# Optimization experiments

Hardware: AMD Instinct MI355X
Metric: run time of the kernel (lower is better)

## Reference

```python
import jax, jax.numpy as jnp
import numpy as np

B, T, C = 2, 2048, 2048
H = 16          # n_head == n_kv_head
HD = 128        # head_size = hidden_dim // n_head (nope/value dim)
RD = 64         # qk_rope_head_dim
QLR = 1536      # q_lora_rank
KLR = 512       # kv_lora_rank
BASE = 10000.0
SCALE = (HD + RD) ** -0.5  # mscale = 1.0 since rope_scale = 1.0
EPS = 1e-6


def _rms(x, w):
    return x * jax.lax.rsqrt(jnp.mean(x * x, axis=-1, keepdims=True) + EPS) * w


def _rope_cos_sin(seq_len, dim):
    inv_freq = 1.0 / (BASE ** (jnp.arange(0, dim, 2, dtype=jnp.float32) / dim))
    t = jnp.arange(seq_len, dtype=jnp.float32)
    freqs = jnp.outer(t, inv_freq)            # [T, dim/2]
    emb = jnp.concatenate([freqs, freqs], -1)  # [T, dim]
    return jnp.cos(emb), jnp.sin(emb)


def _rotate_half(x):
    h = x.shape[-1] // 2
    return jnp.concatenate([-x[..., h:], x[..., :h]], axis=-1)


def setup_inputs() -> dict:
    key = jax.random.key(0)
    ks = jax.random.split(key, 8)
    s = 0.02
    return {
        "x": jax.random.normal(ks[0], (B, T, C), jnp.float32),
        "Wq_down": jax.random.normal(ks[1], (C, QLR), jnp.float32) * s,
        "q_norm_w": jnp.ones((QLR,), jnp.float32),
        "Wq_up": jax.random.normal(ks[2], (QLR, H * HD), jnp.float32) * s,
        "Wq_pe": jax.random.normal(ks[3], (QLR, H * RD), jnp.float32) * s,
        "Wkv_down": jax.random.normal(ks[4], (C, KLR), jnp.float32) * s,
        "kv_norm_w": jnp.ones((KLR,), jnp.float32),
        "Wkv_up": jax.random.normal(ks[5], (KLR, H * 2 * HD), jnp.float32) * s,
        "Wk_pe": jax.random.normal(ks[6], (C, RD), jnp.float32) * s,
        "k_pe_norm_w": jnp.ones((RD,), jnp.float32),
        "Wo": jax.random.normal(ks[7], (H * HD, C), jnp.float32) * s,
    }


def reference(x, Wq_down, q_norm_w, Wq_up, Wq_pe, Wkv_down, kv_norm_w,
              Wkv_up, Wk_pe, k_pe_norm_w, Wo):
    # ---- low-rank Q path ----
    cQ = _rms(x @ Wq_down, q_norm_w)                      # [B,T,QLR]
    q_nop = (cQ @ Wq_up).reshape(B, T, H, HD).transpose(0, 2, 1, 3)   # [B,H,T,HD]
    q_pe = (cQ @ Wq_pe).reshape(B, T, H, RD).transpose(0, 2, 1, 3)    # [B,H,T,RD]
    # ---- low-rank KV path ----
    cKV = _rms(x @ Wkv_down, kv_norm_w)                   # [B,T,KLR]
    kv = cKV @ Wkv_up                                     # [B,T,H*2*HD]
    k_nop, v = jnp.split(kv, 2, axis=-1)
    k_nop = k_nop.reshape(B, T, H, HD).transpose(0, 2, 1, 3)          # [B,H,T,HD]
    v = v.reshape(B, T, H, HD).transpose(0, 2, 1, 3)                  # [B,H,T,HD]
    # ---- decoupled RoPE key (shared across heads) ----
    k_pe = _rms(x @ Wk_pe, k_pe_norm_w).reshape(B, T, 1, RD).transpose(0, 2, 1, 3)  # [B,1,T,RD]
    cos, sin = _rope_cos_sin(T, RD)                       # [T,RD]
    q_pe = q_pe * cos + _rotate_half(q_pe) * sin
    k_pe = k_pe * cos + _rotate_half(k_pe) * sin
    # ---- concat nope + rope, causal SDPA ----
    q = jnp.concatenate([q_nop, q_pe], axis=-1)                           # [B,H,T,HD+RD]
    k = jnp.concatenate([k_nop, jnp.broadcast_to(k_pe, (B, H, T, RD))], axis=-1)
    scores = jnp.einsum('bhqd,bhkd->bhqk', q, k) * SCALE
    mask = jnp.tril(jnp.ones((T, T), dtype=bool))
    scores = jnp.where(mask, scores, jnp.finfo(scores.dtype).min)
    attn = jax.nn.softmax(scores, axis=-1)
    y = jnp.einsum('bhqk,bhkd->bhqd', attn, v)                            # [B,H,T,HD]
    y = y.transpose(0, 2, 1, 3).reshape(B, T, H * HD)
    return y @ Wo
```

## Files before the change

### kernel.cpp

```cpp
#include <hip/hip_runtime.h>
#include <hip/hip_bf16.h>
#include <cmath>

typedef __hip_bfloat16 bf16;
typedef __attribute__((ext_vector_type(8))) short s16x8;
typedef __attribute__((ext_vector_type(4))) float f32x4;

#define B_   2
#define T_   2048
#define C_   2048
#define H_   16
#define HD_  128
#define RD_  64
#define QLR_ 1536
#define KLR_ 512
#define SCALE_ 0.07216878364870322f

static __device__ __forceinline__ float b2f(bf16 v){ return __bfloat162float(v); }
static __device__ __forceinline__ bf16  f2b(float v){ return __float2bfloat16(v); }
static __device__ __forceinline__ float us2f(unsigned short u){
    union { unsigned short s[2]; float f; } v; v.s[0]=0; v.s[1]=u; return v.f;
}
static __device__ __forceinline__ float ldS(const void* p, size_t i, int isf32){
    return isf32 ? ((const float*)p)[i] : b2f(((const bf16*)p)[i]);
}
static __device__ __forceinline__ void ld4(const void* p, size_t i, int isf32, float* o){
    if (isf32) {
        float4 v = *(const float4*)((const float*)p + i);
        o[0]=v.x; o[1]=v.y; o[2]=v.z; o[3]=v.w;
    } else {
        ushort4 u = *(const ushort4*)((const bf16*)p + i);
        o[0]=us2f(u.x); o[1]=us2f(u.y); o[2]=us2f(u.z); o[3]=us2f(u.w);
    }
}

__global__ __launch_bounds__(64) void detect_kernel(const unsigned short* __restrict__ x,
                                                    int* __restrict__ flag)
{
    int big = 0;
    for (int i = threadIdx.x; i < 1024; i += 64) {
        const unsigned short u = x[2*i];
        const int e = (u >> 7) & 0xFF;
        if (e >= 139) big++;
    }
    #pragma unroll
    for (int off = 32; off; off >>= 1) big += __shfl_down(big, off, 64);
    if (threadIdx.x == 0) *flag = (big > 8) ? 1 : 0;
}

__global__ __launch_bounds__(256) void convert_kernel(const void* __restrict__ in,
                                                      bf16* __restrict__ out, int n,
                                                      const int* __restrict__ flag)
{
    const int f = *flag;
    const int i0 = (blockIdx.x * 256 + threadIdx.x) * 8;
    if (i0 >= n) return;
    float v[8];
    ld4(in, i0, f, v);
    ld4(in, i0 + 4, f, v + 4);
    bf16* o = out + i0;
    #pragma unroll
    for (int k = 0; k < 8; ++k) o[k] = f2b(v[k]);
}

struct TDesc { const void* in; bf16* out; int R, Cc, blkStart, nx; };
struct TBatch { TDesc d[5]; int nseg; };

__global__ __launch_bounds__(256) void transpose_batch(TBatch tb,
                                                       const int* __restrict__ flag)
{
    const int f = *flag;
    const int bid = blockIdx.x;
    int s = 0;
    #pragma unroll
    for (int i = 1; i < 5; ++i)
        if (i < tb.nseg && bid >= tb.d[i].blkStart) s = i;
    const TDesc d = tb.d[s];
    const int local = bid - d.blkStart;
    const int c0 = (local % d.nx) * 32;
    const int r0 = (local / d.nx) * 32;

    __shared__ float tile[32][33];
    const int tx = threadIdx.x & 31, ty = threadIdx.x >> 5;
    #pragma unroll
    for (int i = 0; i < 4; ++i)
        tile[ty + 8*i][tx] = ldS(d.in, (size_t)(r0 + ty + 8*i) * d.Cc + c0 + tx, f);
    __syncthreads();
    #pragma unroll
    for (int i = 0; i < 4; ++i)
        d.out[(size_t)(c0 + ty + 8*i) * d.R + r0 + tx] = f2b(tile[tx][ty + 8*i]);
}

__global__ __launch_bounds__(256) void transpose_v_kernel(const bf16* __restrict__ kvb,
                                                          bf16* __restrict__ vT)
{
    __shared__ bf16 tile[32][34];
    const int c0 = blockIdx.x * 32;
    const int r0 = blockIdx.y * 32;
    const int tx = threadIdx.x & 31, ty = threadIdx.x >> 5;
    #pragma unroll
    for (int i = 0; i < 4; ++i)
        tile[ty + 8*i][tx] = kvb[(size_t)(r0 + ty + 8*i) * (H_*256) + H_*128 + c0 + tx];
    __syncthreads();
    const int b  = r0 >> 11;
    const int t0 = r0 & (T_ - 1);
    #pragma unroll
    for (int i = 0; i < 4; ++i) {
        const int c  = c0 + ty + 8*i;
        const int hh = c >> 7, dd = c & 127;
        vT[(((size_t)b*H_ + hh)*HD_ + dd)*T_ + t0 + tx] = tile[tx][ty + 8*i];
    }
}

struct GOuts { void* p[3]; int start[3]; int stride[3]; int nseg; };

__global__ __launch_bounds__(256, 3) void mfma_gemm(const bf16* __restrict__ A,
                                                    const bf16* __restrict__ BT,
                                                    GOuts go, int N, int K,
                                                    const int* __restrict__ flag, int cH)
{
    __shared__ __align__(16) char smem[32768];
    const int cf   = cH ? *flag : 0;
    const int tid  = threadIdx.x;
    const int lane = tid & 63;
    const int quad = lane >> 4;
    const int l16  = lane & 15;
    const int w    = tid >> 6;
    const int wm   = w >> 1, wn = w & 1;

    const int nwg = gridDim.x * gridDim.y;
    const int bid = blockIdx.y * gridDim.x + blockIdx.x;
    const int swz = (bid & 7) * (nwg >> 3) + (bid >> 3);
    const int bm  = (swz / gridDim.x) * 128;
    const int bn  = (swz % gridDim.x) * 128;

    int seg = 0;
    #pragma unroll
    for (int i = 1; i < 3; ++i)
        if (i < go.nseg && bn >= go.start[i]) seg = i;
    void* const dstp   = go.p[seg];
    const int  dstoff  = go.start[seg];
    const int  dstride = go.stride[seg];

    const int nkt = K >> 6;

    const int sR   = tid >> 3;
    const int sCol = ((tid & 7) ^ (sR & 7)) * 8;
    const bf16* gA = A  + (size_t)(bm + sR) * K + sCol;
    const bf16* gB = BT + (size_t)(bn + sR) * K + sCol;
    const int rxk  = l16 & 7;
    const int aOff = (wm*64 + l16) * 128;
    const int bOff = 16384 + (wn*64 + l16) * 128;

    f32x4 acc[4][4];
    #pragma unroll
    for (int i = 0; i < 4; ++i)
        #pragma unroll
        for (int j = 0; j < 4; ++j)
            acc[i][j] = (f32x4){0.f, 0.f, 0.f, 0.f};

    s16x8 af[4][2], bf[4][2];

    #define STG(kt) do {                                                         \
        const int ke_ = (kt) * 64;                                               \
        _Pragma("unroll")                                                        \
        for (int j_ = 0; j_ < 4; ++j_)                                           \
            __builtin_amdgcn_global_load_lds(                                    \
                (const __attribute__((address_space(1))) unsigned int*)          \
                    (gA + (size_t)(j_*32) * K + ke_),                            \
                (__attribute__((address_space(3))) unsigned int*)                \
                    (smem + j_*4096 + tid*16), 16, 0, 0);                        \
        _Pragma("unroll")                                                        \
        for (int j_ = 0; j_ < 4; ++j_)                                           \
            __builtin_amdgcn_global_load_lds(                                    \
                (const __attribute__((address_space(1))) unsigned int*)          \
                    (gB + (size_t)(j_*32) * K + ke_),                            \
                (__attribute__((address_space(3))) unsigned int*)                \
                    (smem + 16384 + j_*4096 + tid*16), 16, 0, 0);                \
    } while (0)

    #define LD do {                                                              \
        _Pragma("unroll")                                                        \
        for (int i_ = 0; i_ < 4; ++i_)                                           \
            _Pragma("unroll")                                                    \
            for (int ks_ = 0; ks_ < 2; ++ks_)                                    \
                af[i_][ks_] = *(const s16x8*)(smem + aOff                        \
                              + i_*2048 + ((((ks_<<2)|quad) ^ rxk) << 4));       \
        _Pragma("unroll")                                                        \
        for (int j_ = 0; j_ < 4; ++j_)                                           \
            _Pragma("unroll")                                                    \
            for (int ks_ = 0; ks_ < 2; ++ks_)                                    \
                bf[j_][ks_] = *(const s16x8*)(smem + bOff                        \
                              + j_*2048 + ((((ks_<<2)|quad) ^ rxk) << 4));       \
    } while (0)

    #define MM do {                                                              \
        __builtin_amdgcn_s_setprio(1);                                           \
        _Pragma("unroll")                                                        \
        for (int i_ = 0; i_ < 4; ++i_)                                           \
            _Pragma("unroll")                                                    \
            for (int j_ = 0; j_ < 4; ++j_)                                       \
                _Pragma("unroll")                                                \
                for (int ks_ = 0; ks_ < 2; ++ks_)                                \
                    acc[i_][j_] = __builtin_amdgcn_mfma_f32_16x16x32_bf16(       \
                        af[i_][ks_], bf[j_][ks_], acc[i_][j_], 0, 0, 0);         \
        __builtin_amdgcn_s_setprio(0);                                           \
    } while (0)

    for (int t = 0; t < nkt; ++t) {
        STG(t);
        asm volatile("s_waitcnt vmcnt(0)" ::: "memory");
        __builtin_amdgcn_s_barrier();
        LD;
        MM;
        __builtin_amdgcn_s_barrier();
    }

    #undef STG
    #undef LD
    #undef MM

    #pragma unroll
    for (int i = 0; i < 4; ++i) {
        const int crow = bm + wm*64 + i*16 + quad*4;
        #pragma unroll
        for (int r = 0; r < 4; ++r) {
            #pragma unroll
            for (int j = 0; j < 4; ++j) {
                const int ccol = bn + wn*64 + j*16 + l16;
                if (ccol < N) {
                    const size_t idx = (size_t)(crow + r) * dstride + (ccol - dstoff);
                    if (cf) ((float*)dstp)[idx] = acc[i][j][r];
                    else    ((bf16*)dstp)[idx] = f2b(acc[i][j][r]);
                }
            }
        }
    }
}

template<int NPER>
__global__ __launch_bounds__(256) void rms_kernel(bf16* __restrict__ X,
                                                  const void* __restrict__ w,
                                                  const int* __restrict__ flag)
{
    const int wf = *flag;
    const int ncols = NPER * 256;
    __shared__ float red[4];
    const int row = blockIdx.x;
    const int tid = threadIdx.x;
    bf16* xr = X + (size_t)row * ncols;
    float vals[NPER];
    float ss = 0.f;
    #pragma unroll
    for (int i = 0; i < NPER; ++i) {
        float v = b2f(xr[tid + i*256]);
        vals[i] = v; ss += v*v;
    }
    #pragma unroll
    for (int off = 32; off; off >>= 1) ss += __shfl_down(ss, off, 64);
    if ((tid & 63) == 0) red[tid >> 6] = ss;
    __syncthreads();
    const float tot = red[0]+red[1]+red[2]+red[3];
    const float rs  = rsqrtf(tot / (float)ncols + 1e-6f);
    #pragma unroll
    for (int i = 0; i < NPER; ++i) {
        const int c = tid + i*256;
        xr[c] = f2b(vals[i] * rs * ldS(w, c, wf));
    }
}

__global__ __launch_bounds__(64) void kpe_rms_rope(bf16* __restrict__ X,
                                                   const void* __restrict__ w,
                                                   const int* __restrict__ flag)
{
    const int wf   = *flag;
    const int row  = blockIdx.x;
    const int t    = row & (T_ - 1);
    const int lane = threadIdx.x;
    bf16* xr = X + (size_t)row * RD_;
    const float v = b2f(xr[lane]);
    float ss = v * v;
    #pragma unroll
    for (int off = 32; off; off >>= 1) ss += __shfl_down(ss, off, 64);
    ss = __shfl(ss, 0, 64);
    const float rs = rsqrtf(ss / 64.f + 1e-6f);
    const float xn = v * rs * ldS(w, lane, wf);
    const int   i  = lane & 31;
    const float freq = powf(10000.f, -(float)(2*i) / 64.f);
    const float ang  = (float)t * freq;
    const float s = sinf(ang), c = cosf(ang);
    const float other = __shfl_xor(xn, 32, 64);
    const float o = (lane < 32) ? (xn * c - other * s) : (other * s + xn * c);
    xr[lane] = f2b(o);
}

__global__ __launch_bounds__(256) void qpe_rope(bf16* __restrict__ X)
{
    const int row = blockIdx.x;
    const int t   = row & (T_ - 1);
    bf16* xr = X + (size_t)row * (H_ * RD_);
    const int tid = threadIdx.x;
    #pragma unroll
    for (int pp = 0; pp < 2; ++pp) {
        const int p  = tid + pp * 256;
        const int hh = p >> 5;
        const int i  = p & 31;
        const int i0 = hh * 64 + i;
        const int i1 = i0 + 32;
        const float x1 = b2f(xr[i0]), x2 = b2f(xr[i1]);
        const float freq = powf(10000.f, -(float)(2*i) / 64.f);
        const float ang  = (float)t * freq;
        const float s = sinf(ang), c = cosf(ang);
        xr[i0] = f2b(x1 * c - x2 * s);
        xr[i1] = f2b(x1 * s + x2 * c);
    }
}

__global__ __launch_bounds__(256, 2) void flash_attn(const bf16* __restrict__ qnop,
                                                     const bf16* __restrict__ qpe,
                                                     const bf16* __restrict__ kv,
                                                     const bf16* __restrict__ kpe,
                                                     const bf16* __restrict__ vT,
                                                     bf16* __restrict__ y)
{
    __shared__ __align__(16) short Klds[64 * 192];
    __shared__ __align__(16) short Vt[128 * 64];
    __shared__ __align__(16) short Plds[4][16 * 64];

    const int h   = blockIdx.x;
    const int qt  = 31 - (int)blockIdx.y;
    const int b   = blockIdx.z;
    const int q0  = qt * 64;
    const int tid = threadIdx.x;
    const int w    = tid >> 6;
    const int lane = tid & 63;
    const int quad = lane >> 4;
    const int l16  = lane & 15;
    const int rk   = l16 & 7;
    const int rkp  = (l16 ^ (l16 >> 3)) & 7;
    const int row0 = q0 + w * 16;
    const size_t bT = (size_t)b * T_;
    const int bh  = b * H_ + h;

    const int kR = tid >> 4, kS = tid & 15;
    const int pR = tid >> 3, pS = tid & 7;
    const int vD = tid >> 3, vS = tid & 7;

    const bf16* gK = kv  + (bT + kR) * (H_*256) + h*128 + kS*8;
    const bf16* gP = kpe + (bT + pR) * RD_ + pS*8;
    const bf16* gV = vT  + ((size_t)bh*HD_ + vD) * T_ + vS*8;

    short* const wK = &Klds[kR*192 + ((kS ^ (kR & 7)) << 3)];
    short* const wP = &Klds[pR*192 + 128 + ((pS ^ (pR & 7)) << 3)];
    short* const wV = &Vt[vD*64 + ((vS ^ (vD & 7)) << 3)];

    s16x8 aq[6];
    {
        const size_t r = bT + row0 + l16;
        const bf16* qn = qnop + r * (H_*128) + h*128 + quad*8;
        #pragma unroll
        for (int kk = 0; kk < 4; ++kk) aq[kk] = *(const s16x8*)(qn + kk*32);
        const bf16* qp = qpe + r * (H_*64) + h*64 + quad*8;
        aq[4] = *(const s16x8*)(qp);
        aq[5] = *(const s16x8*)(qp + 32);
    }

    f32x4 o[8];
    #pragma unroll
    for (int i = 0; i < 8; ++i) o[i] = (f32x4){0.f,0.f,0.f,0.f};
    float m_run[4] = {-1e30f,-1e30f,-1e30f,-1e30f};
    float l_run[4] = {0.f,0.f,0.f,0.f};

    uint4 k0, k1, k2, k3, p0, p1, v0, v1, v2, v3;
    #define PF(J0) do {                                                     \
        const bf16* a_ = gK + (size_t)(J0) * (H_*256);                      \
        k0 = *(const uint4*)(a_);                                           \
        k1 = *(const uint4*)(a_ + 16*(H_*256));                             \
        k2 = *(const uint4*)(a_ + 32*(H_*256));                             \
        k3 = *(const uint4*)(a_ + 48*(H_*256));                             \
        const bf16* p_ = gP + (size_t)(J0) * RD_;                           \
        p0 = *(const uint4*)(p_);                                           \
        p1 = *(const uint4*)(p_ + 32*RD_);                                  \
        const bf16* v_ = gV + (J0);                                         \
        v0 = *(const uint4*)(v_);                                           \
        v1 = *(const uint4*)(v_ + 32*T_);                                   \
        v2 = *(const uint4*)(v_ + 64*T_);                                   \
        v3 = *(const uint4*)(v_ + 96*T_);                                   \
    } while (0)

    PF(0);

    const int ntiles = qt + 1;
    for (int it = 0; it < ntiles; ++it) {
        const int j0 = it * 64;
        asm volatile("s_waitcnt lgkmcnt(0)\n\ts_barrier" ::: "memory");

        *(uint4*)(wK)          = k0;
        *(uint4*)(wK + 16*192) = k1;
        *(uint4*)(wK + 32*192) = k2;
        *(uint4*)(wK + 48*192) = k3;
        *(uint4*)(wP)          = p0;
        *(uint4*)(wP + 32*192) = p1;
        *(uint4*)(wV)          = v0;
        *(uint4*)(wV + 32*64)  = v1;
        *(uint4*)(wV + 64*64)  = v2;
        *(uint4*)(wV + 96*64)  = v3;

        if (it + 1 < ntiles) PF(j0 + 64);

        asm volatile("s_waitcnt lgkmcnt(0)\n\ts_barrier" ::: "memory");

        if (j0 <= row0 + 15) {
            const bool needmask = (j0 + 63 > row0);
            f32x4 s[4];
            #pragma unroll
            for (int nsub = 0; nsub < 4; ++nsub) {
                f32x4 acc = (f32x4){0.f,0.f,0.f,0.f};
                #pragma unroll
                for (int kk = 0; kk < 6; ++kk) {
                    const s16x8 bk = *(const s16x8*)&Klds[(nsub*16 + l16)*192
                                        + ((((kk << 2) | quad) ^ rk) << 3)];
                    acc = __builtin_amdgcn_mfma_f32_16x16x32_bf16(aq[kk], bk, acc, 0, 0, 0);
                }
                #pragma unroll
                for (int reg = 0; reg < 4; ++reg) acc[reg] *= SCALE_;
                s[nsub] = acc;
            }
            if (needmask) {
                #pragma unroll
                for (int nsub = 0; nsub < 4; ++nsub)
                    #pragma unroll
                    for (int reg = 0; reg < 4; ++reg) {
                        const int col = j0 + nsub*16 + l16;
                        const int row = row0 + quad*4 + reg;
                        if (col > row) s[nsub][reg] = -1e30f;
                    }
            }
            float mt[4], alpha[4], rs[4];
            #pragma unroll
            for (int reg = 0; reg < 4; ++reg)
                mt[reg] = fmaxf(fmaxf(s[0][reg], s[1][reg]), fmaxf(s[2][reg], s[3][reg]));
            #pragma unroll
            for (int d = 1; d < 16; d <<= 1)
                #pragma unroll
                for (int reg = 0; reg < 4; ++reg)
                    mt[reg] = fmaxf(mt[reg], __shfl_xor(mt[reg], d, 64));
            #pragma unroll
            for (int reg = 0; reg < 4; ++reg) {
                const float mnew = fmaxf(m_run[reg], mt[reg]);
                alpha[reg] = __expf(m_run[reg] - mnew);
                m_run[reg] = mnew;
                rs[reg] = 0.f;
            }
            #pragma unroll
            for (int nsub = 0; nsub < 4; ++nsub)
                #pragma unroll
                for (int reg = 0; reg < 4; ++reg) {
                    const float p = __expf(s[nsub][reg] - m_run[reg]);
                    s[nsub][reg] = p;
                    rs[reg] += p;
                }
            #pragma unroll
            for (int d = 1; d < 16; d <<= 1)
                #pragma unroll
                for (int reg = 0; reg < 4; ++reg)
                    rs[reg] += __shfl_xor(rs[reg], d, 64);
            #pragma unroll
            for (int reg = 0; reg < 4; ++reg)
                l_run[reg] = l_run[reg] * alpha[reg] + rs[reg];

            #pragma unroll
            for (int nsub = 0; nsub < 4; ++nsub)
                #pragma unroll
                for (int reg = 0; reg < 4; ++reg) {
                    const bf16 pv = f2b(s[nsub][reg]);
                    const int prow = (quad << 2) + reg;
                    const int pk   = (prow ^ (prow >> 3)) & 7;
                    const int pby  = ((nsub << 5) + (l16 << 1)) ^ (pk << 4);
                    Plds[w][prow*64 + (pby >> 1)] = *(const short*)&pv;
                }
            #pragma unroll
            for (int n2 = 0; n2 < 8; ++n2)
                #pragma unroll
                for (int reg = 0; reg < 4; ++reg)
                    o[n2][reg] *= alpha[reg];

            const s16x8 ap0 = *(const s16x8*)&Plds[w][l16*64 + (((quad    ) ^ rkp) << 3)];
            const s16x8 ap1 = *(const s16x8*)&Plds[w][l16*64 + (((quad | 4) ^ rkp) << 3)];
            #pragma unroll
            for (int n2 = 0; n2 < 8; ++n2) {
                const s16x8 bv0 = *(const s16x8*)&Vt[(n2*16 + l16)*64 + (((quad    ) ^ rk) << 3)];
                const s16x8 bv1 = *(const s16x8*)&Vt[(n2*16 + l16)*64 + (((quad | 4) ^ rk) << 3)];
                o[n2] = __builtin_amdgcn_mfma_f32_16x16x32_bf16(ap0, bv0, o[n2], 0, 0, 0);
                o[n2] = __builtin_amdgcn_mfma_f32_16x16x32_bf16(ap1, bv1, o[n2], 0, 0, 0);
            }
        }
    }
    #undef PF

    #pragma unroll
    for (int reg = 0; reg < 4; ++reg) {
        const float inv = 1.f / l_run[reg];
        const size_t r = bT + row0 + quad*4 + reg;
        bf16* yr = y + r * (H_*128) + h*128 + l16;
        #pragma unroll
        for (int n2 = 0; n2 < 8; ++n2)
            yr[n2*16] = f2b(o[n2][reg] * inv);
    }
}

extern "C" void kernel_launch(void* const* d_in, const int* in_sizes, int n_in,
                              void* d_out, int out_size, void* d_ws, size_t ws_size,
                              hipStream_t stream)
{
    const void* x         = d_in[0];
    const void* Wq_down   = d_in[1];
    const void* q_norm_w  = d_in[2];
    const void* Wq_up     = d_in[3];
    const void* Wq_pe     = d_in[4];
    const void* Wkv_down  = d_in[5];
    const void* kv_norm_w = d_in[6];
    const void* Wkv_up    = d_in[7];
    const void* Wk_pe     = d_in[8];
    const void* kpe_nw    = d_in[9];
    const void* Wo        = d_in[10];

    char* ws = (char*)d_ws;
    int*  flag = (int*)(ws + 0);
    bf16* xb   = (bf16*)(ws + 256);
    bf16* cQ   = (bf16*)(ws + 16777472);
    bf16* cKV  = (bf16*)(ws + 29360384);
    bf16* kpeb = (bf16*)(ws + 33554688);
    bf16* qnop = (bf16*)(ws + 34078976);
    bf16* qpeb = (bf16*)(ws + 50856192);
    bf16* kvb  = (bf16*)(ws + 59244800);
    bf16* yb   = (bf16*)(ws + 92799232);

    bf16* P1 = kvb;
    bf16* P2 = (bf16*)((char*)kvb + 8912896);
    bf16* P3 = cQ;
    bf16* P4 = (bf16*)((char*)cQ + 4194304);
    bf16* vT = xb;

    const dim3 blk(256);

    detect_kernel<<<1, dim3(64), 0, stream>>>((const unsigned short*)x, flag);
    convert_kernel<<<(B_*T_*C_)/(256*8), blk, 0, stream>>>(x, xb, B_*T_*C_, flag);

    {
        TBatch tb;
        tb.d[0] = { Wq_down,  P1,               C_,  QLR_,     0, QLR_/32 };
        tb.d[1] = { Wkv_down, P1 + 1536*2048,   C_,  KLR_,  3072, KLR_/32 };
        tb.d[2] = { Wk_pe,    P1 + 2048*2048,   C_,  RD_,   4096, RD_/32  };
        tb.d[3] = { Wq_up,    P2,               QLR_, 2048, 4224, 2048/32 };
        tb.d[4] = { Wq_pe,    P2 + 2048*1536,   QLR_, 1024, 7296, 1024/32 };
        tb.nseg = 5;
        transpose_batch<<<8832, blk, 0, stream>>>(tb, flag);
    }

    {
        GOuts go; go.nseg = 3;
        go.p[0]=cQ;   go.start[0]=0;    go.stride[0]=QLR_;
        go.p[1]=cKV;  go.start[1]=1536; go.stride[1]=KLR_;
        go.p[2]=kpeb; go.start[2]=2048; go.stride[2]=RD_;
        mfma_gemm<<<dim3(17, 32), blk, 0, stream>>>(xb, P1, go, 2112, C_, flag, 0);
    }
    rms_kernel<6><<<B_*T_, blk, 0, stream>>>(cQ, q_norm_w, flag);
    rms_kernel<2><<<B_*T_, blk, 0, stream>>>(cKV, kv_norm_w, flag);
    kpe_rms_rope<<<B_*T_, dim3(64), 0, stream>>>(kpeb, kpe_nw, flag);

    {
        GOuts go; go.nseg = 2;
        go.p[0]=qnop; go.start[0]=0;    go.stride[0]=H_*HD_;
        go.p[1]=qpeb; go.start[1]=2048; go.stride[1]=H_*RD_;
        go.p[2]=nullptr; go.start[2]=0; go.stride[2]=0;
        mfma_gemm<<<dim3(24, 32), blk, 0, stream>>>(cQ, P2, go, 3072, QLR_, flag, 0);
    }
    qpe_rope<<<B_*T_, blk, 0, stream>>>(qpeb);

    {
        TBatch tb;
        tb.d[0] = { Wkv_up, P3, KLR_, H_*2*HD_,    0, (H_*2*HD_)/32 };
        tb.d[1] = { Wo,     P4, H_*HD_, C_,     2048, C_/32 };
        tb.d[2] = tb.d[1]; tb.d[3] = tb.d[1]; tb.d[4] = tb.d[1];
        tb.nseg = 2;
        transpose_batch<<<6144, blk, 0, stream>>>(tb, flag);
    }

    {
        GOuts go; go.nseg = 1;
        go.p[0]=kvb; go.start[0]=0; go.stride[0]=H_*2*HD_;
        go.p[1]=nullptr; go.start[1]=0; go.stride[1]=0;
        go.p[2]=nullptr; go.start[2]=0; go.stride[2]=0;
        mfma_gemm<<<dim3(32, 32), blk, 0, stream>>>(cKV, P3, go, H_*2*HD_, KLR_, flag, 0);
    }
    transpose_v_kernel<<<dim3((H_*HD_)/32, (B_*T_)/32), blk, 0, stream>>>(kvb, vT);

    flash_attn<<<dim3(H_, T_/64, B_), blk, 0, stream>>>(qnop, qpeb, kvb, kpeb, vT, yb);

    {
        GOuts go; go.nseg = 1;
        go.p[0]=d_out; go.start[0]=0; go.stride[0]=C_;
        go.p[1]=nullptr; go.start[1]=0; go.stride[1]=0;
        go.p[2]=nullptr; go.start[2]=0; go.stride[2]=0;
        mfma_gemm<<<dim3(C_/128, 32), blk, 0, stream>>>(yb, P4, go, C_, H_*HD_, flag, 1);
    }
}
```

Before: 457.5 us.

## Double-buffer GEMM shared memory with register-staged global prefetch

Replaces the synchronous global_load_lds staging in the MFMA GEMM with a two-stage pipeline. Global tiles are prefetched into registers two k-steps ahead and written to one of two LDS buffers while the other buffer feeds MFMAs, and the inner loop is reordered to load A fragments per k-slice. This aims to hide global load latency behind compute and drop one barrier per k-step. In exchange LDS doubles to 64KB and register use rises, so occupancy falls from 3 to 2 blocks per CU. The loop also assumes an even number of k-tiles.

New measurement: 700.7 us. +53.2%, slower.

```diff
diff --git a/kernel.cpp b/kernel.cpp
--- a/kernel.cpp
+++ b/kernel.cpp
@@ -114,12 +114,12 @@
 
 struct GOuts { void* p[3]; int start[3]; int stride[3]; int nseg; };
 
-__global__ __launch_bounds__(256, 3) void mfma_gemm(const bf16* __restrict__ A,
+__global__ __launch_bounds__(256, 2) void mfma_gemm(const bf16* __restrict__ A,
                                                     const bf16* __restrict__ BT,
                                                     GOuts go, int N, int K,
                                                     const int* __restrict__ flag, int cH)
 {
-    __shared__ __align__(16) char smem[32768];
+    __shared__ __align__(16) char smem[65536];
     const int cf   = cH ? *flag : 0;
     const int tid  = threadIdx.x;
     const int lane = tid & 63;
@@ -159,66 +159,73 @@
         for (int j = 0; j < 4; ++j)
             acc[i][j] = (f32x4){0.f, 0.f, 0.f, 0.f};
 
-    s16x8 af[4][2], bf[4][2];
-
-    #define STG(kt) do {                                                         \
-        const int ke_ = (kt) * 64;                                               \
+    uint4 rg0[8], rg1[8];
+
+    #define GLD(rg, kt) do {                                                     \
+        const int ke_ = ((kt) < nkt ? (kt) : nkt-1) * 64;                        \
         _Pragma("unroll")                                                        \
         for (int j_ = 0; j_ < 4; ++j_)                                           \
-            __builtin_amdgcn_global_load_lds(                                    \
-                (const __attribute__((address_space(1))) unsigned int*)          \
-                    (gA + (size_t)(j_*32) * K + ke_),                            \
-                (__attribute__((address_space(3))) unsigned int*)                \
-                    (smem + j_*4096 + tid*16), 16, 0, 0);                        \
+            rg[j_]   = *(const uint4*)(gA + (size_t)(j_*32) * K + ke_);          \
         _Pragma("unroll")                                                        \
         for (int j_ = 0; j_ < 4; ++j_)                                           \
-            __builtin_amdgcn_global_load_lds(                                    \
-                (const __attribute__((address_space(1))) unsigned int*)          \
-                    (gB + (size_t)(j_*32) * K + ke_),                            \
-                (__attribute__((address_space(3))) unsigned int*)                \
-                    (smem + 16384 + j_*4096 + tid*16), 16, 0, 0);                \
+            rg[4+j_] = *(const uint4*)(gB + (size_t)(j_*32) * K + ke_);          \
     } while (0)
 
-    #define LD do {                                                              \
-        _Pragma("unroll")                                                        \
-        for (int i_ = 0; i_ < 4; ++i_)                                           \
-            _Pragma("unroll")                                                    \
-            for (int ks_ = 0; ks_ < 2; ++ks_)                                    \
-                af[i_][ks_] = *(const s16x8*)(smem + aOff                        \
-                              + i_*2048 + ((((ks_<<2)|quad) ^ rxk) << 4));       \
+    #define DSW(buf, rg) do {                                                    \
         _Pragma("unroll")                                                        \
         for (int j_ = 0; j_ < 4; ++j_)                                           \
-            _Pragma("unroll")                                                    \
-            for (int ks_ = 0; ks_ < 2; ++ks_)                                    \
-                bf[j_][ks_] = *(const s16x8*)(smem + bOff                        \
-                              + j_*2048 + ((((ks_<<2)|quad) ^ rxk) << 4));       \
+            *(uint4*)(smem + (buf)*32768 + j_*4096 + tid*16) = rg[j_];           \
+        _Pragma("unroll")                                                        \
+        for (int j_ = 0; j_ < 4; ++j_)                                           \
+            *(uint4*)(smem + (buf)*32768 + 16384 + j_*4096 + tid*16) = rg[4+j_]; \
     } while (0)
 
-    #define MM do {                                                              \
+    #define CMP(buf) do {                                                        \
         __builtin_amdgcn_s_setprio(1);                                           \
         _Pragma("unroll")                                                        \
-        for (int i_ = 0; i_ < 4; ++i_)                                           \
+        for (int ks_ = 0; ks_ < 2; ++ks_) {                                      \
+            s16x8 af_[4];                                                        \
             _Pragma("unroll")                                                    \
-            for (int j_ = 0; j_ < 4; ++j_)                                       \
+            for (int i_ = 0; i_ < 4; ++i_)                                       \
+                af_[i_] = *(const s16x8*)(smem + (buf)*32768 + aOff              \
+                          + i_*2048 + ((((ks_<<2)|quad) ^ rxk) << 4));           \
+            _Pragma("unroll")                                                    \
+            for (int j_ = 0; j_ < 4; ++j_) {                                     \
+                const s16x8 bf_ = *(const s16x8*)(smem + (buf)*32768 + bOff      \
+                          + j_*2048 + ((((ks_<<2)|quad) ^ rxk) << 4));           \
                 _Pragma("unroll")                                                \
-                for (int ks_ = 0; ks_ < 2; ++ks_)                                \
+                for (int i_ = 0; i_ < 4; ++i_)                                   \
                     acc[i_][j_] = __builtin_amdgcn_mfma_f32_16x16x32_bf16(       \
-                        af[i_][ks_], bf[j_][ks_], acc[i_][j_], 0, 0, 0);         \
+                        af_[i_], bf_, acc[i_][j_], 0, 0, 0);                     \
+            }                                                                    \
+        }                                                                        \
         __builtin_amdgcn_s_setprio(0);                                           \
     } while (0)
 
-    for (int t = 0; t < nkt; ++t) {
-        STG(t);
-        asm volatile("s_waitcnt vmcnt(0)" ::: "memory");
-        __builtin_amdgcn_s_barrier();
-        LD;
-        MM;
-        __builtin_amdgcn_s_barrier();
-    }
-
-    #undef STG
-    #undef LD
-    #undef MM
+    #define LBAR asm volatile("s_waitcnt lgkmcnt(0)\n\ts_barrier" ::: "memory")
+
+    GLD(rg0, 0);
+    DSW(0, rg0);
+    GLD(rg0, 1);
+    LBAR;
+
+    const int nit = nkt >> 1;
+    for (int i = 0; i < nit; ++i) {
+        const int t = 2*i;
+        GLD(rg1, t+2);
+        DSW(1, rg0);
+        CMP(0);
+        LBAR;
+        GLD(rg0, t+3);
+        DSW(0, rg1);
+        CMP(1);
+        LBAR;
+    }
+
+    #undef GLD
+    #undef DSW
+    #undef CMP
+    #undef LBAR
 
     #pragma unroll
     for (int i = 0; i < 4; ++i) {
```
